# Kernel optimization log

Measured on AMD Instinct MI355X. Metric: run time of the kernel, lower is better.

The kernel has to match this reference:

```python
import jax, jax.numpy as jnp
from jax import lax
import numpy as np

# Module hyperparameters (match init_kwargs)
N = 4            # number of multiplex cells per feature map
NUM_FM = 64      # feature maps in the input
NF = N * NUM_FM  # lateral channel count = 256
H = W = 32       # feature map height/width
D = 2            # lateral neighborhood radius
PRD = 2          # padding repair distance (must equal D for symmetric pad)
KS = 2 * D + 1   # lateral kernel size = 5
IOTA = 0.1       # blend of activation vs lateral support for winner selection
B = 16           # batch size


def minmax_fm(x):
    """Min-max normalize each feature map (over the last two dims) to [0,1].
    Degenerate (constant) maps map to 0."""
    mn = jnp.min(x, axis=(-2, -1), keepdims=True)
    mx = jnp.max(x, axis=(-2, -1), keepdims=True)
    denom = mx - mn
    safe = jnp.where(denom > 0, denom, 1.0)
    return jnp.where(denom > 0, (x - mn) / safe, 0.0)


def _pad(A):
    # pad_activations: zeros of shape (.., PRD+D+H, PRD+D+W), A at [PRD:-PRD]
    # with PRD == D this is symmetric (PRD, D) padding.
    return jnp.pad(A, ((0, 0), (0, 0), (PRD, D), (PRD, D)))


def _conv(x, w):
    # x: (B, Cin, H', W'), w: (Cout, Cin, KS, KS) -> VALID conv (padding=0)
    return lax.conv_general_dilated(x, w, (1, 1), 'VALID',
                                    dimension_numbers=('NCHW', 'OIHW', 'NCHW'))


def setup_inputs() -> dict:
    key = jax.random.key(0)
    k1, k2 = jax.random.split(key)
    A = jax.random.uniform(k1, (B, NUM_FM, H, W), dtype=jnp.float32)
    K = jax.random.normal(k2, (NF, NF, KS, KS), dtype=jnp.float32)  # trained lateral kernel
    S = jnp.ones((NF,), dtype=jnp.float32)                          # scaling param
    return {"A": A, "K": K, "S": S}


def reference(A, K, S):
    batch = A.shape[0]
    # A.repeat(1, n, 1, 1): tile input n times along channels -> (B, NF, H, W)
    A_rep = jnp.tile(A, (1, N, 1, 1))

    # First lateral pass: conv with minmax-normalized K^T, scaled by S, minmaxed.
    L1 = _conv(_pad(A_rep), minmax_fm(jnp.swapaxes(K, 0, 1))) / NUM_FM
    L1 = L1 * S[None, :, None, None]
    L1 = minmax_fm(L1)

    # Winner-take-all multiplex selection (deterministic branch):
    s = jnp.sum((1.0 - IOTA) * A_rep + IOTA * L1, axis=(-2, -1))  # (B, NF)
    s = jnp.swapaxes(s.reshape(batch, N, NUM_FM), 1, 2)            # (B, NUM_FM, N)
    A_max = jnp.argmax(s, axis=-1)                                  # (B, NUM_FM)
    fm_idx = NUM_FM * A_max + jnp.arange(NUM_FM)                    # (B, NUM_FM) channel ids

    # Active-channel mask (complement = inactive_multiplex_idx in the original)
    active = jnp.zeros((batch, NF), dtype=bool)
    active = active.at[jnp.arange(batch)[:, None], fm_idx].set(True)

    # Zero inactive channels of A (tmp_A) and diagonal K[i,i] for inactive i
    # (large_K[b, idx, idx] = 0 is pairwise/diagonal fancy indexing in torch).
    tmp_A = A_rep * active[:, :, None, None].astype(A_rep.dtype)
    eye = jnp.eye(NF, dtype=bool)
    kill = eye[None, :, :] & (~active)[:, :, None]                  # (B, NF, NF)
    large_K = jnp.where(kill[..., None, None], 0.0, K[None])        # (B, NF, NF, KS, KS)

    # Second lateral pass: per-sample conv with per-sample kernel.
    pA = _pad(tmp_A)

    def per_sample(x, Kb):
        w = minmax_fm(jnp.swapaxes(Kb, 0, 1))
        return _conv(x[None], w)[0]

    L2 = jax.vmap(per_sample)(pA, large_K) / NUM_FM                 # (B, NF, H, W)

    # Gather winning channels: filtered_L (B, NUM_FM, H, W)
    return jnp.take_along_axis(L2, fm_idx[:, :, None, None], axis=1)
```

## Files before the change

### kernel.cpp

```cpp
#include <hip/hip_runtime.h>


#define NFM 64
#define NMX 4
#define NFC 256
#define HW 1024
#define KK 25

typedef unsigned short u16;
typedef short short8 __attribute__((ext_vector_type(8)));
typedef float f32x4 __attribute__((ext_vector_type(4)));

__device__ __forceinline__ u16 f2bfbits(float f) {
    unsigned int u = __float_as_uint(f);
    u += 0x7fffu + ((u >> 16) & 1u);
    return (u16)(u >> 16);
}
__device__ __forceinline__ float bf2f(u16 v) {
    return __uint_as_float(((unsigned int)v) << 16);
}

__global__ __launch_bounds__(256) void kw(const float* __restrict__ K,
                                          char* __restrict__ Wpk) {
    __shared__ float wlds[16 * 16 * KK];
    int gq = blockIdx.x, ot = blockIdx.y, t = threadIdx.x;
    int tg = t >> 4, to = t & 15;
    int g = gq * 16 + tg, o = ot * 16 + to;

    float wacc[KK];
#pragma unroll
    for (int k = 0; k < KK; ++k) wacc[k] = 0.f;
#pragma unroll
    for (int n = 0; n < NMX; ++n) {
        const float* src = K + ((n * NFM + g) * NFC + o) * KK;
        float v[KK];
        float mn = 1e30f, mx = -1e30f;
#pragma unroll
        for (int k = 0; k < KK; ++k) {
            v[k] = src[k];
            mn = fminf(mn, v[k]);
            mx = fmaxf(mx, v[k]);
        }
        float d = mx - mn;
        float r = d > 0.f ? 1.f / d : 0.f;
#pragma unroll
        for (int k = 0; k < KK; ++k) wacc[k] += (v[k] - mn) * r;
    }
#pragma unroll
    for (int k = 0; k < KK; ++k) wlds[(tg * 16 + to) * KK + k] = wacc[k];
    __syncthreads();

    int gh = gq >> 1;
    for (int idx = t; idx < KK * 32; idx += 256) {
        int dydx = idx >> 5, l32 = idx & 31;
        int quad = (gq & 1) * 2 + (l32 >> 4);
        int oo = l32 & 15;
        int l = quad * 16 + oo;
        short8 hs, ls;
#pragma unroll
        for (int j = 0; j < 8; ++j) {
            int gl = (l32 >> 4) * 8 + j;
            float v = wlds[(gl * 16 + oo) * KK + dydx];
            u16 h = f2bfbits(v);
            hs[j] = (short)h;
            ls[j] = (short)f2bfbits(v - bf2f(h));
        }
        char* cb = Wpk + (ot * 50 + dydx * 2 + gh) * 2048 + l * 16;
        *(short8*)cb = hs;
        *(short8*)(cb + 1024) = ls;
    }
}

#define MFMA6(P, BH, BL)                                                             \
    acc[0][P] = __builtin_amdgcn_mfma_f32_16x16x32_bf16(cah0, BH, acc[0][P], 0, 0, 0); \
    acc[1][P] = __builtin_amdgcn_mfma_f32_16x16x32_bf16(cah1, BH, acc[1][P], 0, 0, 0); \
    acc[0][P] = __builtin_amdgcn_mfma_f32_16x16x32_bf16(cah0, BL, acc[0][P], 0, 0, 0); \
    acc[1][P] = __builtin_amdgcn_mfma_f32_16x16x32_bf16(cah1, BL, acc[1][P], 0, 0, 0); \
    acc[0][P] = __builtin_amdgcn_mfma_f32_16x16x32_bf16(cal0, BH, acc[0][P], 0, 0, 0); \
    acc[1][P] = __builtin_amdgcn_mfma_f32_16x16x32_bf16(cal1, BH, acc[1][P], 0, 0, 0);

__global__ __launch_bounds__(512, 2) void kscore(const float* __restrict__ A,
                                                 const char* __restrict__ Wpk,
                                                 float4* __restrict__ part) {
    __shared__ u16 slabh[6 * 36 * 72];
    __shared__ u16 slabl[6 * 36 * 72];
    int t = threadIdx.x;
    int y2 = blockIdx.x, b = blockIdx.y;
    int y0 = y2 * 2;
    int lane = t & 63;
    int wv = __builtin_amdgcn_readfirstlane(t >> 6);
    int n15 = lane & 15, quad = lane >> 4;

    const float* Ab = A + b * NFM * HW;
    for (int ry = 0; ry < 6; ++ry) {
        int gy = y0 - 2 + ry;
        bool rowok = (gy >= 0) && (gy < 32);
        for (int c = 0; c < 5; ++c) {
            int id2 = c * 512 + t;
            if (id2 < 2304) {
                int g = (id2 * 3641) >> 17;
                int xi = id2 - g * 36;
                float v = 0.f;
                if (rowok && xi >= 2 && xi < 34)
                    v = Ab[g * HW + gy * 32 + xi - 2];
                u16 h = f2bfbits(v);
                u16 l = f2bfbits(v - bf2f(h));
                int idx = (ry * 36 + xi) * 72 + g;
                slabh[idx] = h;
                slabl[idx] = l;
            }
        }
    }
    __syncthreads();

    f32x4 acc[2][4];
#pragma unroll
    for (int m = 0; m < 2; ++m)
#pragma unroll
        for (int p = 0; p < 4; ++p)
#pragma unroll
            for (int r = 0; r < 4; ++r) acc[m][p][r] = 0.f;

    const char* wbase0 = Wpk + (wv * 2) * 50 * 2048 + lane * 16;
    const char* wbase1 = wbase0 + 50 * 2048;
    short8 cah0 = *(const short8*)(wbase0);
    short8 cal0 = *(const short8*)(wbase0 + 1024);
    short8 cah1 = *(const short8*)(wbase1);
    short8 cal1 = *(const short8*)(wbase1 + 1024);

    int rb0 = n15 * 72 + quad * 8;
    const u16* sh0 = slabh + rb0;
    const u16* sl0 = slabl + rb0;
    short8 bh0 = *(const short8*)(sh0);
    short8 bl0 = *(const short8*)(sl0);
    short8 bh1 = *(const short8*)(sh0 + 16 * 72);
    short8 bl1 = *(const short8*)(sl0 + 16 * 72);
    short8 bh2 = *(const short8*)(sh0 + 36 * 72);
    short8 bl2 = *(const short8*)(sl0 + 36 * 72);
    short8 bh3 = *(const short8*)(sh0 + 52 * 72);
    short8 bl3 = *(const short8*)(sl0 + 52 * 72);

    for (int ks = 0; ks < 50; ++ks) {
        int ksn = ks < 49 ? ks + 1 : 49;
        const char* nb0 = wbase0 + (ksn << 11);
        const char* nb1 = wbase1 + (ksn << 11);
        short8 nah0 = *(const short8*)nb0;
        short8 nal0 = *(const short8*)(nb0 + 1024);
        short8 nah1 = *(const short8*)nb1;
        short8 nal1 = *(const short8*)(nb1 + 1024);
        int dydxn = ksn >> 1;
        int ghn = (ksn & 1) * 32;
        int dyn = dydxn / 5, dxn = dydxn - dyn * 5;
        int rbn = (dyn * 36 + n15 + dxn) * 72 + ghn + quad * 8;
        const u16* shn = slabh + rbn;
        const u16* sln = slabl + rbn;
        short8 nh0 = *(const short8*)(shn);
        short8 nl0 = *(const short8*)(sln);
        short8 nh1 = *(const short8*)(shn + 16 * 72);
        short8 nl1 = *(const short8*)(sln + 16 * 72);
        short8 nh2 = *(const short8*)(shn + 36 * 72);
        short8 nl2 = *(const short8*)(sln + 36 * 72);
        short8 nh3 = *(const short8*)(shn + 52 * 72);
        short8 nl3 = *(const short8*)(sln + 52 * 72);
        __builtin_amdgcn_sched_barrier(0);

        MFMA6(0, bh0, bl0)
        MFMA6(1, bh1, bl1)
        MFMA6(2, bh2, bl2)
        MFMA6(3, bh3, bl3)

        bh0 = nh0; bl0 = nl0; bh1 = nh1; bl1 = nl1;
        bh2 = nh2; bl2 = nl2; bh3 = nh3; bl3 = nl3;
        cah0 = nah0; cal0 = nal0; cah1 = nah1; cal1 = nal1;
    }

#pragma unroll
    for (int m = 0; m < 2; ++m) {
#pragma unroll
        for (int reg = 0; reg < 4; ++reg) {
            float v0 = acc[m][0][reg], v1 = acc[m][1][reg];
            float v2 = acc[m][2][reg], v3 = acc[m][3][reg];
            float mn = fminf(fminf(v0, v1), fminf(v2, v3));
            float mx = fmaxf(fmaxf(v0, v1), fmaxf(v2, v3));
            float sm = (v0 + v1) + (v2 + v3);
#pragma unroll
            for (int msk = 1; msk <= 8; msk <<= 1) {
                mn = fminf(mn, __shfl_xor(mn, msk, 64));
                mx = fmaxf(mx, __shfl_xor(mx, msk, 64));
                sm += __shfl_xor(sm, msk, 64);
            }
            if (n15 == 0) {
                int o = (wv * 2 + m) * 16 + quad * 4 + reg;
                part[(b * NFC + o) * 16 + y2] = make_float4(mn, mx, sm, 0.f);
            }
        }
    }
}

__global__ __launch_bounds__(256) void kpackO(const float* __restrict__ K,
                                              const float4* __restrict__ part,
                                              const float* __restrict__ S,
                                              char* __restrict__ Wob) {
    __shared__ float scl[NFC];
    __shared__ int igL[NFM];
    __shared__ __align__(16) char cbuf[25 * 2048];
    int ft = blockIdx.x, b = blockIdx.y, half = blockIdx.z;
    int t = threadIdx.x;
    {
        const float4* pp = part + (b * NFC + t) * 16;
        float mn = 1e30f, mx = -1e30f, sm = 0.f;
#pragma unroll
        for (int r = 0; r < 16; ++r) {
            float4 p = pp[r];
            mn = fminf(mn, p.x);
            mx = fmaxf(mx, p.y);
            sm += p.z;
        }
        float s = S[t] * (1.f / 64.f);
        float mnv = (s >= 0.f ? mn : mx) * s;
        float mxv = (s >= 0.f ? mx : mn) * s;
        float smv = sm * s;
        float d = mxv - mnv;
        scl[t] = d > 0.f ? (smv - 1024.f * mnv) / d : 0.f;
    }
    __syncthreads();
    if (t < NFM) {
        float best = scl[t];
        int bi = 0;
#pragma unroll
        for (int n = 1; n < NMX; ++n) {
            float v = scl[n * NFM + t];
            if (v > best) { best = v; bi = n; }
        }
        igL[t] = bi * NFM + t;
    }
    __syncthreads();

    int g32 = t & 31, fh = t >> 5;
    int quad = g32 >> 3, j = g32 & 7;
    char* wdst = Wob + b * 409600 + ft * 102400;

    int i = igL[half * 32 + g32];
#pragma unroll
    for (int e = 0; e < 2; ++e) {
        int f15 = fh * 2 + e;
        int o = igL[ft * 16 + f15];
        const float* src = K + (i * NFC + o) * KK;
        float v[KK];
        float mn = 1e30f, mx = -1e30f;
#pragma unroll
        for (int k = 0; k < KK; ++k) {
            v[k] = src[k];
            mn = fminf(mn, v[k]);
            mx = fmaxf(mx, v[k]);
        }
        float d = mx - mn;
        float r = d > 0.f ? 1.f / d : 0.f;
        char* base = cbuf + (quad * 16 + f15) * 16 + j * 2;
#pragma unroll
        for (int k = 0; k < KK; ++k) {
            float nv = (v[k] - mn) * r;
            u16 h = f2bfbits(nv);
            u16 l = f2bfbits(nv - bf2f(h));
            *(u16*)(base + k * 2048) = h;
            *(u16*)(base + k * 2048 + 1024) = l;
        }
    }
    __syncthreads();
    for (int idx = t; idx < 3200; idx += 256) {
        int ch = idx >> 7, w = idx & 127;
        *(float4*)(wdst + (ch * 2 + half) * 2048 + w * 16) =
            *(const float4*)(cbuf + ch * 2048 + w * 16);
    }
}

__global__ __launch_bounds__(256, 4) void kout(const float* __restrict__ A,
                                               const char* __restrict__ Wob,
                                               float* __restrict__ out) {
    __shared__ u16 slabh[6 * 20 * 72];
    __shared__ u16 slabl[6 * 20 * 72];
    int t = threadIdx.x;
    int xh = blockIdx.x, yb2 = blockIdx.y, b = blockIdx.z;
    int y0 = yb2 * 2, x0 = xh * 16;
    int lane = t & 63;
    int wv = __builtin_amdgcn_readfirstlane(t >> 6);
    int n15 = lane & 15, quad = lane >> 4;

    const float* Ab = A + b * NFM * HW;
    for (int ry = 0; ry < 6; ++ry) {
        int gy = y0 - 2 + ry;
        bool rowok = (gy >= 0) && (gy < 32);
        for (int c = 0; c < 5; ++c) {
            int id2 = c * 256 + t;
            int g = (id2 * 6554) >> 17;
            int xi = id2 - g * 20;
            int x = x0 + xi - 2;
            float v = 0.f;
            if (rowok && x >= 0 && x < 32)
                v = Ab[g * HW + gy * 32 + x];
            u16 h = f2bfbits(v);
            u16 l = f2bfbits(v - bf2f(h));
            int idx = (ry * 20 + xi) * 72 + g;
            slabh[idx] = h;
            slabl[idx] = l;
        }
    }
    __syncthreads();

    f32x4 acc[2];
#pragma unroll
    for (int r = 0; r < 2; ++r)
#pragma unroll
        for (int jr = 0; jr < 4; ++jr) acc[r][jr] = 0.f;

    const char* wbase = Wob + b * 409600 + (wv * 50) * 2048 + lane * 16;
    short8 cah = *(const short8*)(wbase);
    short8 cal = *(const short8*)(wbase + 1024);

    int rb0 = n15 * 72 + quad * 8;
    short8 bh0 = *(const short8*)(slabh + rb0);
    short8 bl0 = *(const short8*)(slabl + rb0);
    short8 bh1 = *(const short8*)(slabh + rb0 + 20 * 72);
    short8 bl1 = *(const short8*)(slabl + rb0 + 20 * 72);

    for (int ks = 0; ks < 50; ++ks) {
        int ksn = ks < 49 ? ks + 1 : 49;
        const char* nb = wbase + (ksn << 11);
        short8 nah = *(const short8*)nb;
        short8 nal = *(const short8*)(nb + 1024);

        int dydxn = ksn >> 1;
        int ghn = (ksn & 1) * 32;
        int dyn = dydxn / 5, dxn = dydxn - dyn * 5;
        int rbn = (dyn * 20 + n15 + dxn) * 72 + ghn + quad * 8;
        short8 nh0 = *(const short8*)(slabh + rbn);
        short8 nl0 = *(const short8*)(slabl + rbn);
        short8 nh1 = *(const short8*)(slabh + rbn + 20 * 72);
        short8 nl1 = *(const short8*)(slabl + rbn + 20 * 72);
        __builtin_amdgcn_sched_barrier(0);

        acc[0] = __builtin_amdgcn_mfma_f32_16x16x32_bf16(cah, bh0, acc[0], 0, 0, 0);
        acc[1] = __builtin_amdgcn_mfma_f32_16x16x32_bf16(cah, bh1, acc[1], 0, 0, 0);
        acc[0] = __builtin_amdgcn_mfma_f32_16x16x32_bf16(cah, bl0, acc[0], 0, 0, 0);
        acc[1] = __builtin_amdgcn_mfma_f32_16x16x32_bf16(cah, bl1, acc[1], 0, 0, 0);
        acc[0] = __builtin_amdgcn_mfma_f32_16x16x32_bf16(cal, bh0, acc[0], 0, 0, 0);
        acc[1] = __builtin_amdgcn_mfma_f32_16x16x32_bf16(cal, bh1, acc[1], 0, 0, 0);

        bh0 = nh0; bl0 = nl0; bh1 = nh1; bl1 = nl1;
        cah = nah;
        cal = nal;
    }

#pragma unroll
    for (int r = 0; r < 2; ++r)
#pragma unroll
        for (int reg = 0; reg < 4; ++reg) {
            int f = wv * 16 + quad * 4 + reg;
            out[(b * NFM + f) * HW + (y0 + r) * 32 + x0 + n15] = acc[r][reg] * (1.f / 64.f);
        }
}

extern "C" void kernel_launch(void* const* d_in, const int* in_sizes, int n_in,
                              void* d_out, int out_size, void* d_ws, size_t ws_size,
                              hipStream_t stream) {
    const float* A = (const float*)d_in[0];
    const float* K = (const float*)d_in[1];
    const float* S = (const float*)d_in[2];
    float* out = (float*)d_out;

    char* ws = (char*)d_ws;
    char*   Wob   = ws;
    char*   Wpk   = ws;
    float4* part  = (float4*)(ws + 6553600);

    kw<<<dim3(4, 16), dim3(256), 0, stream>>>(K, Wpk);
    kscore<<<dim3(16, 16), dim3(512), 0, stream>>>(A, Wpk, part);
    kpackO<<<dim3(4, 16, 2), dim3(256), 0, stream>>>(K, part, S, Wob);
    kout<<<dim3(2, 16, 16), dim3(256), 0, stream>>>(A, Wob, out);
}
```

Measured before the change: 141.7 us.

## Fuse four kernels into one cooperative kernel with grid syncs

Merges the weight-pack, score, per-sample weight-pack and output convolution kernels into a single cooperative launch of 256 blocks of 512 threads, separated by grid.sync barriers. This removes three kernel launch gaps and inter-kernel drain. The output stage is remapped to 512-thread blocks with a full 36-wide slab. Phases that used many smaller blocks now run on fewer or partially idle blocks, and each grid barrier adds its own cost. Wpk and Wob alias the same workspace, so correctness depends on the grid syncs ordering the reads and writes.

New measurement: 239.7 us. 1.69x slower.

```diff
diff --git a/kernel.cpp b/kernel.cpp
--- a/kernel.cpp
+++ b/kernel.cpp
@@ -1,4 +1,7 @@
 #include <hip/hip_runtime.h>
+#include <hip/hip_cooperative_groups.h>
+
+namespace cg = cooperative_groups;
 
 
 #define NFM 64
@@ -20,57 +23,6 @@
     return __uint_as_float(((unsigned int)v) << 16);
 }
 
-__global__ __launch_bounds__(256) void kw(const float* __restrict__ K,
-                                          char* __restrict__ Wpk) {
-    __shared__ float wlds[16 * 16 * KK];
-    int gq = blockIdx.x, ot = blockIdx.y, t = threadIdx.x;
-    int tg = t >> 4, to = t & 15;
-    int g = gq * 16 + tg, o = ot * 16 + to;
-
-    float wacc[KK];
-#pragma unroll
-    for (int k = 0; k < KK; ++k) wacc[k] = 0.f;
-#pragma unroll
-    for (int n = 0; n < NMX; ++n) {
-        const float* src = K + ((n * NFM + g) * NFC + o) * KK;
-        float v[KK];
-        float mn = 1e30f, mx = -1e30f;
-#pragma unroll
-        for (int k = 0; k < KK; ++k) {
-            v[k] = src[k];
-            mn = fminf(mn, v[k]);
-            mx = fmaxf(mx, v[k]);
-        }
-        float d = mx - mn;
-        float r = d > 0.f ? 1.f / d : 0.f;
-#pragma unroll
-        for (int k = 0; k < KK; ++k) wacc[k] += (v[k] - mn) * r;
-    }
-#pragma unroll
-    for (int k = 0; k < KK; ++k) wlds[(tg * 16 + to) * KK + k] = wacc[k];
-    __syncthreads();
-
-    int gh = gq >> 1;
-    for (int idx = t; idx < KK * 32; idx += 256) {
-        int dydx = idx >> 5, l32 = idx & 31;
-        int quad = (gq & 1) * 2 + (l32 >> 4);
-        int oo = l32 & 15;
-        int l = quad * 16 + oo;
-        short8 hs, ls;
-#pragma unroll
-        for (int j = 0; j < 8; ++j) {
-            int gl = (l32 >> 4) * 8 + j;
-            float v = wlds[(gl * 16 + oo) * KK + dydx];
-            u16 h = f2bfbits(v);
-            hs[j] = (short)h;
-            ls[j] = (short)f2bfbits(v - bf2f(h));
-        }
-        char* cb = Wpk + (ot * 50 + dydx * 2 + gh) * 2048 + l * 16;
-        *(short8*)cb = hs;
-        *(short8*)(cb + 1024) = ls;
-    }
-}
-
 #define MFMA6(P, BH, BL)                                                             \
     acc[0][P] = __builtin_amdgcn_mfma_f32_16x16x32_bf16(cah0, BH, acc[0][P], 0, 0, 0); \
     acc[1][P] = __builtin_amdgcn_mfma_f32_16x16x32_bf16(cah1, BH, acc[1][P], 0, 0, 0); \
@@ -79,285 +31,343 @@
     acc[0][P] = __builtin_amdgcn_mfma_f32_16x16x32_bf16(cal0, BH, acc[0][P], 0, 0, 0); \
     acc[1][P] = __builtin_amdgcn_mfma_f32_16x16x32_bf16(cal1, BH, acc[1][P], 0, 0, 0);
 
-__global__ __launch_bounds__(512, 2) void kscore(const float* __restrict__ A,
-                                                 const char* __restrict__ Wpk,
-                                                 float4* __restrict__ part) {
-    __shared__ u16 slabh[6 * 36 * 72];
-    __shared__ u16 slabl[6 * 36 * 72];
+__global__ __launch_bounds__(512, 1) void kfused(const float* __restrict__ A,
+                                                 const float* __restrict__ K,
+                                                 const float* __restrict__ S,
+                                                 char* __restrict__ Wpk,
+                                                 char* __restrict__ Wob,
+                                                 float4* __restrict__ part,
+                                                 float* __restrict__ out) {
+    __shared__ __align__(16) char smem[62464];
+    cg::grid_group grid = cg::this_grid();
     int t = threadIdx.x;
-    int y2 = blockIdx.x, b = blockIdx.y;
-    int y0 = y2 * 2;
+    int bid = blockIdx.y * 16 + blockIdx.x;
     int lane = t & 63;
     int wv = __builtin_amdgcn_readfirstlane(t >> 6);
     int n15 = lane & 15, quad = lane >> 4;
 
-    const float* Ab = A + b * NFM * HW;
-    for (int ry = 0; ry < 6; ++ry) {
-        int gy = y0 - 2 + ry;
-        bool rowok = (gy >= 0) && (gy < 32);
-        for (int c = 0; c < 5; ++c) {
-            int id2 = c * 512 + t;
-            if (id2 < 2304) {
-                int g = (id2 * 3641) >> 17;
-                int xi = id2 - g * 36;
-                float v = 0.f;
-                if (rowok && xi >= 2 && xi < 34)
-                    v = Ab[g * HW + gy * 32 + xi - 2];
+    if (bid < 64) {
+        float* wlds = (float*)smem;
+        int gq = bid & 3, ot = bid >> 2;
+        if (t < 256) {
+            int tg = t >> 4, to = t & 15;
+            int g = gq * 16 + tg, o = ot * 16 + to;
+            float wacc[KK];
+#pragma unroll
+            for (int k = 0; k < KK; ++k) wacc[k] = 0.f;
+#pragma unroll
+            for (int n = 0; n < NMX; ++n) {
+                const float* src = K + ((n * NFM + g) * NFC + o) * KK;
+                float v[KK];
+                float mn = 1e30f, mx = -1e30f;
+#pragma unroll
+                for (int k = 0; k < KK; ++k) {
+                    v[k] = src[k];
+                    mn = fminf(mn, v[k]);
+                    mx = fmaxf(mx, v[k]);
+                }
+                float d = mx - mn;
+                float r = d > 0.f ? 1.f / d : 0.f;
+#pragma unroll
+                for (int k = 0; k < KK; ++k) wacc[k] += (v[k] - mn) * r;
+            }
+#pragma unroll
+            for (int k = 0; k < KK; ++k) wlds[(tg * 16 + to) * KK + k] = wacc[k];
+        }
+        __syncthreads();
+        int gh = gq >> 1;
+        for (int idx = t; idx < KK * 32; idx += 512) {
+            int dydx = idx >> 5, l32 = idx & 31;
+            int qd = (gq & 1) * 2 + (l32 >> 4);
+            int oo = l32 & 15;
+            int l = qd * 16 + oo;
+            short8 hs, ls;
+#pragma unroll
+            for (int j = 0; j < 8; ++j) {
+                int gl = (l32 >> 4) * 8 + j;
+                float v = wlds[(gl * 16 + oo) * KK + dydx];
                 u16 h = f2bfbits(v);
-                u16 l = f2bfbits(v - bf2f(h));
-                int idx = (ry * 36 + xi) * 72 + g;
-                slabh[idx] = h;
-                slabl[idx] = l;
-            }
+                hs[j] = (short)h;
+                ls[j] = (short)f2bfbits(v - bf2f(h));
+            }
+            char* cb = Wpk + (ot * 50 + dydx * 2 + gh) * 2048 + l * 16;
+            *(short8*)cb = hs;
+            *(short8*)(cb + 1024) = ls;
         }
     }
-    __syncthreads();
-
-    f32x4 acc[2][4];
-#pragma unroll
-    for (int m = 0; m < 2; ++m)
-#pragma unroll
-        for (int p = 0; p < 4; ++p)
-#pragma unroll
-            for (int r = 0; r < 4; ++r) acc[m][p][r] = 0.f;
-
-    const char* wbase0 = Wpk + (wv * 2) * 50 * 2048 + lane * 16;
-    const char* wbase1 = wbase0 + 50 * 2048;
-    short8 cah0 = *(const short8*)(wbase0);
-    short8 cal0 = *(const short8*)(wbase0 + 1024);
-    short8 cah1 = *(const short8*)(wbase1);
-    short8 cal1 = *(const short8*)(wbase1 + 1024);
-
-    int rb0 = n15 * 72 + quad * 8;
-    const u16* sh0 = slabh + rb0;
-    const u16* sl0 = slabl + rb0;
-    short8 bh0 = *(const short8*)(sh0);
-    short8 bl0 = *(const short8*)(sl0);
-    short8 bh1 = *(const short8*)(sh0 + 16 * 72);
-    short8 bl1 = *(const short8*)(sl0 + 16 * 72);
-    short8 bh2 = *(const short8*)(sh0 + 36 * 72);
-    short8 bl2 = *(const short8*)(sl0 + 36 * 72);
-    short8 bh3 = *(const short8*)(sh0 + 52 * 72);
-    short8 bl3 = *(const short8*)(sl0 + 52 * 72);
-
-    for (int ks = 0; ks < 50; ++ks) {
-        int ksn = ks < 49 ? ks + 1 : 49;
-        const char* nb0 = wbase0 + (ksn << 11);
-        const char* nb1 = wbase1 + (ksn << 11);
-        short8 nah0 = *(const short8*)nb0;
-        short8 nal0 = *(const short8*)(nb0 + 1024);
-        short8 nah1 = *(const short8*)nb1;
-        short8 nal1 = *(const short8*)(nb1 + 1024);
-        int dydxn = ksn >> 1;
-        int ghn = (ksn & 1) * 32;
-        int dyn = dydxn / 5, dxn = dydxn - dyn * 5;
-        int rbn = (dyn * 36 + n15 + dxn) * 72 + ghn + quad * 8;
-        const u16* shn = slabh + rbn;
-        const u16* sln = slabl + rbn;
-        short8 nh0 = *(const short8*)(shn);
-        short8 nl0 = *(const short8*)(sln);
-        short8 nh1 = *(const short8*)(shn + 16 * 72);
-        short8 nl1 = *(const short8*)(sln + 16 * 72);
-        short8 nh2 = *(const short8*)(shn + 36 * 72);
-        short8 nl2 = *(const short8*)(sln + 36 * 72);
-        short8 nh3 = *(const short8*)(shn + 52 * 72);
-        short8 nl3 = *(const short8*)(sln + 52 * 72);
-        __builtin_amdgcn_sched_barrier(0);
-
-        MFMA6(0, bh0, bl0)
-        MFMA6(1, bh1, bl1)
-        MFMA6(2, bh2, bl2)
-        MFMA6(3, bh3, bl3)
-
-        bh0 = nh0; bl0 = nl0; bh1 = nh1; bl1 = nl1;
-        bh2 = nh2; bl2 = nl2; bh3 = nh3; bl3 = nl3;
-        cah0 = nah0; cal0 = nal0; cah1 = nah1; cal1 = nal1;
+    grid.sync();
+
+    {
+        u16* slabh = (u16*)smem;
+        u16* slabl = slabh + 6 * 36 * 72;
+        int y2 = blockIdx.x, b = blockIdx.y;
+        int y0 = y2 * 2;
+
+        const float* Ab = A + b * NFM * HW;
+        for (int ry = 0; ry < 6; ++ry) {
+            int gy = y0 - 2 + ry;
+            bool rowok = (gy >= 0) && (gy < 32);
+            for (int c = 0; c < 5; ++c) {
+                int id2 = c * 512 + t;
+                if (id2 < 2304) {
+                    int g = (id2 * 3641) >> 17;
+                    int xi = id2 - g * 36;
+                    float v = 0.f;
+                    if (rowok && xi >= 2 && xi < 34)
+                        v = Ab[g * HW + gy * 32 + xi - 2];
+                    u16 h = f2bfbits(v);
+                    u16 l = f2bfbits(v - bf2f(h));
+                    int idx = (ry * 36 + xi) * 72 + g;
+                    slabh[idx] = h;
+                    slabl[idx] = l;
+                }
+            }
+        }
+        __syncthreads();
+
+        f32x4 acc[2][4];
+#pragma unroll
+        for (int m = 0; m < 2; ++m)
+#pragma unroll
+            for (int p = 0; p < 4; ++p)
+#pragma unroll
+                for (int r = 0; r < 4; ++r) acc[m][p][r] = 0.f;
+
+        const char* wbase0 = Wpk + (wv * 2) * 50 * 2048 + lane * 16;
+        const char* wbase1 = wbase0 + 50 * 2048;
+        short8 cah0 = *(const short8*)(wbase0);
+        short8 cal0 = *(const short8*)(wbase0 + 1024);
+        short8 cah1 = *(const short8*)(wbase1);
+        short8 cal1 = *(const short8*)(wbase1 + 1024);
+
+        int rb0 = n15 * 72 + quad * 8;
+        const u16* sh0 = slabh + rb0;
+        const u16* sl0 = slabl + rb0;
+        short8 bh0 = *(const short8*)(sh0);
+        short8 bl0 = *(const short8*)(sl0);
+        short8 bh1 = *(const short8*)(sh0 + 16 * 72);
+        short8 bl1 = *(const short8*)(sl0 + 16 * 72);
+        short8 bh2 = *(const short8*)(sh0 + 36 * 72);
+        short8 bl2 = *(const short8*)(sl0 + 36 * 72);
+        short8 bh3 = *(const short8*)(sh0 + 52 * 72);
+        short8 bl3 = *(const short8*)(sl0 + 52 * 72);
+
+        for (int ks = 0; ks < 50; ++ks) {
+            int ksn = ks < 49 ? ks + 1 : 49;
+            const char* nb0 = wbase0 + (ksn << 11);
+            const char* nb1 = wbase1 + (ksn << 11);
+            short8 nah0 = *(const short8*)nb0;
+            short8 nal0 = *(const short8*)(nb0 + 1024);
+            short8 nah1 = *(const short8*)nb1;
+            short8 nal1 = *(const short8*)(nb1 + 1024);
+            int dydxn = ksn >> 1;
+            int ghn = (ksn & 1) * 32;
+            int dyn = dydxn / 5, dxn = dydxn - dyn * 5;
+            int rbn = (dyn * 36 + n15 + dxn) * 72 + ghn + quad * 8;
+            const u16* shn = slabh + rbn;
+            const u16* sln = slabl + rbn;
+            short8 nh0 = *(const short8*)(shn);
+            short8 nl0 = *(const short8*)(sln);
+            short8 nh1 = *(const short8*)(shn + 16 * 72);
+            short8 nl1 = *(const short8*)(sln + 16 * 72);
+            short8 nh2 = *(const short8*)(shn + 36 * 72);
+            short8 nl2 = *(const short8*)(sln + 36 * 72);
+            short8 nh3 = *(const short8*)(shn + 52 * 72);
+            short8 nl3 = *(const short8*)(sln + 52 * 72);
+            __builtin_amdgcn_sched_barrier(0);
+
+            MFMA6(0, bh0, bl0)
+            MFMA6(1, bh1, bl1)
+            MFMA6(2, bh2, bl2)
+            MFMA6(3, bh3, bl3)
+
+            bh0 = nh0; bl0 = nl0; bh1 = nh1; bl1 = nl1;
+            bh2 = nh2; bl2 = nl2; bh3 = nh3; bl3 = nl3;
+            cah0 = nah0; cal0 = nal0; cah1 = nah1; cal1 = nal1;
+        }
+
+#pragma unroll
+        for (int m = 0; m < 2; ++m) {
+#pragma unroll
+            for (int reg = 0; reg < 4; ++reg) {
+                float v0 = acc[m][0][reg], v1 = acc[m][1][reg];
+                float v2 = acc[m][2][reg], v3 = acc[m][3][reg];
+                float mn = fminf(fminf(v0, v1), fminf(v2, v3));
+                float mx = fmaxf(fmaxf(v0, v1), fmaxf(v2, v3));
+                float sm = (v0 + v1) + (v2 + v3);
+#pragma unroll
+                for (int msk = 1; msk <= 8; msk <<= 1) {
+                    mn = fminf(mn, __shfl_xor(mn, msk, 64));
+                    mx = fmaxf(mx, __shfl_xor(mx, msk, 64));
+                    sm += __shfl_xor(sm, msk, 64);
+                }
+                if (n15 == 0) {
+                    int o = (wv * 2 + m) * 16 + quad * 4 + reg;
+                    part[(b * NFC + o) * 16 + y2] = make_float4(mn, mx, sm, 0.f);
+                }
+            }
+        }
     }
-
-#pragma unroll
-    for (int m = 0; m < 2; ++m) {
-#pragma unroll
-        for (int reg = 0; reg < 4; ++reg) {
-            float v0 = acc[m][0][reg], v1 = acc[m][1][reg];
-            float v2 = acc[m][2][reg], v3 = acc[m][3][reg];
-            float mn = fminf(fminf(v0, v1), fminf(v2, v3));
-            float mx = fmaxf(fmaxf(v0, v1), fmaxf(v2, v3));
-            float sm = (v0 + v1) + (v2 + v3);
-#pragma unroll
-            for (int msk = 1; msk <= 8; msk <<= 1) {
-                mn = fminf(mn, __shfl_xor(mn, msk, 64));
-                mx = fmaxf(mx, __shfl_xor(mx, msk, 64));
-                sm += __shfl_xor(sm, msk, 64);
-            }
-            if (n15 == 0) {
-                int o = (wv * 2 + m) * 16 + quad * 4 + reg;
-                part[(b * NFC + o) * 16 + y2] = make_float4(mn, mx, sm, 0.f);
-            }
+    grid.sync();
+
+    if (bid < 128) {
+        float* scl = (float*)smem;
+        int* igL = (int*)(smem + 1024);
+        char* cbuf = smem + 2048;
+        int ft = bid & 3, b = (bid >> 2) & 15, half = bid >> 6;
+        if (t < 256) {
+            const float4* pp = part + (b * NFC + t) * 16;
+            float mn = 1e30f, mx = -1e30f, sm = 0.f;
+#pragma unroll
+            for (int r = 0; r < 16; ++r) {
+                float4 p = pp[r];
+                mn = fminf(mn, p.x);
+                mx = fmaxf(mx, p.y);
+                sm += p.z;
+            }
+            float s = S[t] * (1.f / 64.f);
+            float mnv = (s >= 0.f ? mn : mx) * s;
+            float mxv = (s >= 0.f ? mx : mn) * s;
+            float smv = sm * s;
+            float d = mxv - mnv;
+            scl[t] = d > 0.f ? (smv - 1024.f * mnv) / d : 0.f;
+        }
+        __syncthreads();
+        if (t < NFM) {
+            float best = scl[t];
+            int bi = 0;
+#pragma unroll
+            for (int n = 1; n < NMX; ++n) {
+                float v = scl[n * NFM + t];
+                if (v > best) { best = v; bi = n; }
+            }
+            igL[t] = bi * NFM + t;
+        }
+        __syncthreads();
+
+        char* wdst = Wob + b * 409600 + ft * 102400;
+        if (t < 256) {
+            int g32 = t & 31, fh = t >> 5;
+            int qd = g32 >> 3, j = g32 & 7;
+            int i = igL[half * 32 + g32];
+#pragma unroll
+            for (int e = 0; e < 2; ++e) {
+                int f15 = fh * 2 + e;
+                int o = igL[ft * 16 + f15];
+                const float* src = K + (i * NFC + o) * KK;
+                float v[KK];
+                float mn = 1e30f, mx = -1e30f;
+#pragma unroll
+                for (int k = 0; k < KK; ++k) {
+                    v[k] = src[k];
+                    mn = fminf(mn, v[k]);
+                    mx = fmaxf(mx, v[k]);
+                }
+                float d = mx - mn;
+                float r = d > 0.f ? 1.f / d : 0.f;
+                char* base = cbuf + (qd * 16 + f15) * 16 + j * 2;
+#pragma unroll
+                for (int k = 0; k < KK; ++k) {
+                    float nv = (v[k] - mn) * r;
+                    u16 h = f2bfbits(nv);
+                    u16 l = f2bfbits(nv - bf2f(h));
+                    *(u16*)(base + k * 2048) = h;
+                    *(u16*)(base + k * 2048 + 1024) = l;
+                }
+            }
+        }
+        __syncthreads();
+        for (int idx = t; idx < 3200; idx += 512) {
+            int ch = idx >> 7, w = idx & 127;
+            *(float4*)(wdst + (ch * 2 + half) * 2048 + w * 16) =
+                *(const float4*)(cbuf + ch * 2048 + w * 16);
         }
     }
-}
-
-__global__ __launch_bounds__(256) void kpackO(const float* __restrict__ K,
-                                              const float4* __restrict__ part,
-                                              const float* __restrict__ S,
-                                              char* __restrict__ Wob) {
-    __shared__ float scl[NFC];
-    __shared__ int igL[NFM];
-    __shared__ __align__(16) char cbuf[25 * 2048];
-    int ft = blockIdx.x, b = blockIdx.y, half = blockIdx.z;
-    int t = threadIdx.x;
+    grid.sync();
+
     {
-        const float4* pp = part + (b * NFC + t) * 16;
-        float mn = 1e30f, mx = -1e30f, sm = 0.f;
-#pragma unroll
-        for (int r = 0; r < 16; ++r) {
-            float4 p = pp[r];
-            mn = fminf(mn, p.x);
-            mx = fmaxf(mx, p.y);
-            sm += p.z;
-        }
-        float s = S[t] * (1.f / 64.f);
-        float mnv = (s >= 0.f ? mn : mx) * s;
-        float mxv = (s >= 0.f ? mx : mn) * s;
-        float smv = sm * s;
-        float d = mxv - mnv;
-        scl[t] = d > 0.f ? (smv - 1024.f * mnv) / d : 0.f;
+        u16* slabh = (u16*)smem;
+        u16* slabl = slabh + 6 * 36 * 72;
+        int yb2 = blockIdx.x, b = blockIdx.y;
+        int y0 = yb2 * 2;
+        int ftile = wv & 3, xh = wv >> 2;
+        int xoff = xh * 16;
+
+        const float* Ab = A + b * NFM * HW;
+        for (int ry = 0; ry < 6; ++ry) {
+            int gy = y0 - 2 + ry;
+            bool rowok = (gy >= 0) && (gy < 32);
+            for (int c = 0; c < 5; ++c) {
+                int id2 = c * 512 + t;
+                if (id2 < 2304) {
+                    int g = (id2 * 3641) >> 17;
+                    int xi = id2 - g * 36;
+                    float v = 0.f;
+                    if (rowok && xi >= 2 && xi < 34)
+                        v = Ab[g * HW + gy * 32 + xi - 2];
+                    u16 h = f2bfbits(v);
+                    u16 l = f2bfbits(v - bf2f(h));
+                    int idx = (ry * 36 + xi) * 72 + g;
+                    slabh[idx] = h;
+                    slabl[idx] = l;
+                }
+            }
+        }
+        __syncthreads();
+
+        f32x4 acc2[2];
+#pragma unroll
+        for (int r = 0; r < 2; ++r)
+#pragma unroll
+            for (int jr = 0; jr < 4; ++jr) acc2[r][jr] = 0.f;
+
+        const char* wbase = Wob + b * 409600 + (ftile * 50) * 2048 + lane * 16;
+        short8 cah = *(const short8*)(wbase);
+        short8 cal = *(const short8*)(wbase + 1024);
+
+        int rb0 = (xoff + n15) * 72 + quad * 8;
+        short8 bh0 = *(const short8*)(slabh + rb0);
+        short8 bl0 = *(const short8*)(slabl + rb0);
+        short8 bh1 = *(const short8*)(slabh + rb0 + 36 * 72);
+        short8 bl1 = *(const short8*)(slabl + rb0 + 36 * 72);
+
+        for (int ks = 0; ks < 50; ++ks) {
+            int ksn = ks < 49 ? ks + 1 : 49;
+            const char* nb = wbase + (ksn << 11);
+            short8 nah = *(const short8*)nb;
+            short8 nal = *(const short8*)(nb + 1024);
+
+            int dydxn = ksn >> 1;
+            int ghn = (ksn & 1) * 32;
+            int dyn = dydxn / 5, dxn = dydxn - dyn * 5;
+            int rbn = (dyn * 36 + xoff + n15 + dxn) * 72 + ghn + quad * 8;
+            short8 nh0 = *(const short8*)(slabh + rbn);
+            short8 nl0 = *(const short8*)(slabl + rbn);
+            short8 nh1 = *(const short8*)(slabh + rbn + 36 * 72);
+            short8 nl1 = *(const short8*)(slabl + rbn + 36 * 72);
+            __builtin_amdgcn_sched_barrier(0);
+
+            acc2[0] = __builtin_amdgcn_mfma_f32_16x16x32_bf16(cah, bh0, acc2[0], 0, 0, 0);
+            acc2[1] = __builtin_amdgcn_mfma_f32_16x16x32_bf16(cah, bh1, acc2[1], 0, 0, 0);
+            acc2[0] = __builtin_amdgcn_mfma_f32_16x16x32_bf16(cah, bl0, acc2[0], 0, 0, 0);
+            acc2[1] = __builtin_amdgcn_mfma_f32_16x16x32_bf16(cah, bl1, acc2[1], 0, 0, 0);
+            acc2[0] = __builtin_amdgcn_mfma_f32_16x16x32_bf16(cal, bh0, acc2[0], 0, 0, 0);
+            acc2[1] = __builtin_amdgcn_mfma_f32_16x16x32_bf16(cal, bh1, acc2[1], 0, 0, 0);
+
+            bh0 = nh0; bl0 = nl0; bh1 = nh1; bl1 = nl1;
+            cah = nah;
+            cal = nal;
+        }
+
+#pragma unroll
+        for (int r = 0; r < 2; ++r)
+#pragma unroll
+            for (int reg = 0; reg < 4; ++reg) {
+                int f = ftile * 16 + quad * 4 + reg;
+                out[(b * NFM + f) * HW + (y0 + r) * 32 + xoff + n15] =
+                    acc2[r][reg] * (1.f / 64.f);
+            }
     }
-    __syncthreads();
-    if (t < NFM) {
-        float best = scl[t];
-        int bi = 0;
-#pragma unroll
-        for (int n = 1; n < NMX; ++n) {
-            float v = scl[n * NFM + t];
-            if (v > best) { best = v; bi = n; }
-        }
-        igL[t] = bi * NFM + t;
-    }
-    __syncthreads();
-
-    int g32 = t & 31, fh = t >> 5;
-    int quad = g32 >> 3, j = g32 & 7;
-    char* wdst = Wob + b * 409600 + ft * 102400;
-
-    int i = igL[half * 32 + g32];
-#pragma unroll
-    for (int e = 0; e < 2; ++e) {
-        int f15 = fh * 2 + e;
-        int o = igL[ft * 16 + f15];
-        const float* src = K + (i * NFC + o) * KK;
-        float v[KK];
-        float mn = 1e30f, mx = -1e30f;
-#pragma unroll
-        for (int k = 0; k < KK; ++k) {
-            v[k] = src[k];
-            mn = fminf(mn, v[k]);
-            mx = fmaxf(mx, v[k]);
-        }
-        float d = mx - mn;
-        float r = d > 0.f ? 1.f / d : 0.f;
-        char* base = cbuf + (quad * 16 + f15) * 16 + j * 2;
-#pragma unroll
-        for (int k = 0; k < KK; ++k) {
-            float nv = (v[k] - mn) * r;
-            u16 h = f2bfbits(nv);
-            u16 l = f2bfbits(nv - bf2f(h));
-            *(u16*)(base + k * 2048) = h;
-            *(u16*)(base + k * 2048 + 1024) = l;
-        }
-    }
-    __syncthreads();
-    for (int idx = t; idx < 3200; idx += 256) {
-        int ch = idx >> 7, w = idx & 127;
-        *(float4*)(wdst + (ch * 2 + half) * 2048 + w * 16) =
-            *(const float4*)(cbuf + ch * 2048 + w * 16);
-    }
-}
-
-__global__ __launch_bounds__(256, 4) void kout(const float* __restrict__ A,
-                                               const char* __restrict__ Wob,
-                                               float* __restrict__ out) {
-    __shared__ u16 slabh[6 * 20 * 72];
-    __shared__ u16 slabl[6 * 20 * 72];
-    int t = threadIdx.x;
-    int xh = blockIdx.x, yb2 = blockIdx.y, b = blockIdx.z;
-    int y0 = yb2 * 2, x0 = xh * 16;
-    int lane = t & 63;
-    int wv = __builtin_amdgcn_readfirstlane(t >> 6);
-    int n15 = lane & 15, quad = lane >> 4;
-
-    const float* Ab = A + b * NFM * HW;
-    for (int ry = 0; ry < 6; ++ry) {
-        int gy = y0 - 2 + ry;
-        bool rowok = (gy >= 0) && (gy < 32);
-        for (int c = 0; c < 5; ++c) {
-            int id2 = c * 256 + t;
-            int g = (id2 * 6554) >> 17;
-            int xi = id2 - g * 20;
-            int x = x0 + xi - 2;
-            float v = 0.f;
-            if (rowok && x >= 0 && x < 32)
-                v = Ab[g * HW + gy * 32 + x];
-            u16 h = f2bfbits(v);
-            u16 l = f2bfbits(v - bf2f(h));
-            int idx = (ry * 20 + xi) * 72 + g;
-            slabh[idx] = h;
-            slabl[idx] = l;
-        }
-    }
-    __syncthreads();
-
-    f32x4 acc[2];
-#pragma unroll
-    for (int r = 0; r < 2; ++r)
-#pragma unroll
-        for (int jr = 0; jr < 4; ++jr) acc[r][jr] = 0.f;
-
-    const char* wbase = Wob + b * 409600 + (wv * 50) * 2048 + lane * 16;
-    short8 cah = *(const short8*)(wbase);
-    short8 cal = *(const short8*)(wbase + 1024);
-
-    int rb0 = n15 * 72 + quad * 8;
-    short8 bh0 = *(const short8*)(slabh + rb0);
-    short8 bl0 = *(const short8*)(slabl + rb0);
-    short8 bh1 = *(const short8*)(slabh + rb0 + 20 * 72);
-    short8 bl1 = *(const short8*)(slabl + rb0 + 20 * 72);
-
-    for (int ks = 0; ks < 50; ++ks) {
-        int ksn = ks < 49 ? ks + 1 : 49;
-        const char* nb = wbase + (ksn << 11);
-        short8 nah = *(const short8*)nb;
-        short8 nal = *(const short8*)(nb + 1024);
-
-        int dydxn = ksn >> 1;
-        int ghn = (ksn & 1) * 32;
-        int dyn = dydxn / 5, dxn = dydxn - dyn * 5;
-        int rbn = (dyn * 20 + n15 + dxn) * 72 + ghn + quad * 8;
-        short8 nh0 = *(const short8*)(slabh + rbn);
-        short8 nl0 = *(const short8*)(slabl + rbn);
-        short8 nh1 = *(const short8*)(slabh + rbn + 20 * 72);
-        short8 nl1 = *(const short8*)(slabl + rbn + 20 * 72);
-        __builtin_amdgcn_sched_barrier(0);
-
-        acc[0] = __builtin_amdgcn_mfma_f32_16x16x32_bf16(cah, bh0, acc[0], 0, 0, 0);
-        acc[1] = __builtin_amdgcn_mfma_f32_16x16x32_bf16(cah, bh1, acc[1], 0, 0, 0);
-        acc[0] = __builtin_amdgcn_mfma_f32_16x16x32_bf16(cah, bl0, acc[0], 0, 0, 0);
-        acc[1] = __builtin_amdgcn_mfma_f32_16x16x32_bf16(cah, bl1, acc[1], 0, 0, 0);
-        acc[0] = __builtin_amdgcn_mfma_f32_16x16x32_bf16(cal, bh0, acc[0], 0, 0, 0);
-        acc[1] = __builtin_amdgcn_mfma_f32_16x16x32_bf16(cal, bh1, acc[1], 0, 0, 0);
-
-        bh0 = nh0; bl0 = nl0; bh1 = nh1; bl1 = nl1;
-        cah = nah;
-        cal = nal;
-    }
-
-#pragma unroll
-    for (int r = 0; r < 2; ++r)
-#pragma unroll
-        for (int reg = 0; reg < 4; ++reg) {
-            int f = wv * 16 + quad * 4 + reg;
-            out[(b * NFM + f) * HW + (y0 + r) * 32 + x0 + n15] = acc[r][reg] * (1.f / 64.f);
-        }
 }
 
 extern "C" void kernel_launch(void* const* d_in, const int* in_sizes, int n_in,
@@ -373,8 +383,7 @@
     char*   Wpk   = ws;
     float4* part  = (float4*)(ws + 6553600);
 
-    kw<<<dim3(4, 16), dim3(256), 0, stream>>>(K, Wpk);
-    kscore<<<dim3(16, 16), dim3(512), 0, stream>>>(A, Wpk, part);
-    kpackO<<<dim3(4, 16, 2), dim3(256), 0, stream>>>(K, part, S, Wob);
-    kout<<<dim3(2, 16, 16), dim3(256), 0, stream>>>(A, Wob, out);
+    void* args[] = {(void*)&A, (void*)&K, (void*)&S, (void*)&Wpk,
+                    (void*)&Wob, (void*)&part, (void*)&out};
+    hipLaunchCooperativeKernel((void*)kfused, dim3(16, 16), dim3(512), args, 0, stream);
 }
```
